# Optimization experiments

Hardware: AMD Instinct MI355X
Metric: run time of the kernel (lower is better)

Reference implementation:

```python
import jax, jax.numpy as jnp
import numpy as np

RADIUS = 0.05
HMIN = -0.02
HMAX = 0.04
NSAMPLE = 64


def setup_inputs() -> dict:
    key = jax.random.key(0)
    k1, k2, k3, k4 = jax.random.split(key, 4)
    B, N, P, C = 2, 16384, 1024, 256
    xyz = jax.random.uniform(k1, (B, N, 3), dtype=jnp.float32)
    new_xyz = jax.random.uniform(k2, (B, P, 3), dtype=jnp.float32)
    rot = jax.random.normal(k3, (B, P, 3, 3), dtype=jnp.float32)
    features = jax.random.normal(k4, (B, C, N), dtype=jnp.float32)
    return {"xyz": xyz, "new_xyz": new_xyz, "rot": rot, "features": features}


def cylinder_query(xyz, new_xyz, rot):
    """Returns (B, P, NSAMPLE) int32 indices into the N axis of xyz.

    Faithful to the torch version: the torch code sorts all N candidates by
    distance (knn with K=N) and then top-k's a cylinder score over them; since
    the candidate set is all N points, this equals a direct top-k of the score
    over N (candidate ordering only affects float ties).
    """
    # delta = candidate point - center, in world frame: (B, P, N, 3)
    delta = xyz[:, None, :, :] - new_xyz[:, :, None, :]
    # rotate into cylinder frame: matmul(delta, rot^T) -> sum_d delta_d * rot[j, d]
    dcyl = jnp.einsum('bpnd,bpjd->bpnj', delta, rot)
    x, y, z = dcyl[..., 0], dcyl[..., 1], dcyl[..., 2]
    radial = jnp.sqrt(jnp.maximum(y * y + z * z, 0.0))
    in_cyl = (radial <= RADIUS) & (x >= HMIN) & (x <= HMAX)
    score = jnp.where(in_cyl, radial + 1e-3 * jnp.abs(x), jnp.inf)
    # smallest-score top-k via top_k on negated score
    neg_vals, pos = jax.lax.top_k(-score, NSAMPLE)  # (B, P, NSAMPLE)
    vals = -neg_vals
    # fallback: nearest point (torch uses idx_cand[..., 0], the KNN-nearest)
    d2 = jnp.sum(delta * delta, axis=-1)  # (B, P, N)
    fallback = jnp.argmin(d2, axis=-1)  # (B, P)
    no_valid = jnp.isinf(vals[..., 0])  # no point inside cylinder
    idx = jnp.where(no_valid[..., None], fallback[..., None], pos)
    return idx


def reference(xyz, new_xyz, rot, features):
    B = xyz.shape[0]
    idx = cylinder_query(xyz, new_xyz, rot)  # (B, P, S)
    # group xyz: (B, P, S, 3)
    grouped_xyz = jax.vmap(lambda p, i: p[i])(xyz, idx)
    grouped_xyz = grouped_xyz - new_xyz[:, :, None, :]
    # rotate_xyz: grouped @ rot  -> sum_d g_d * rot[d, e]
    grouped_xyz = jnp.einsum('bpsd,bpde->bpse', grouped_xyz, rot)
    grouped_xyz = jnp.transpose(grouped_xyz, (0, 3, 1, 2))  # (B, 3, P, S)
    # group features: (B, C, P, S)
    grouped_feat = jax.vmap(lambda f, i: f[:, i])(features, idx)
    return jnp.concatenate([grouped_xyz, grouped_feat], axis=1)  # (B, 3+C, P, S)
```

## Files before the change

kernel.cpp:

```cpp
#include <hip/hip_runtime.h>
#include <stdint.h>

#define B_ 2
#define N_ 16384
#define P_ 1024
#define C_ 256
#define S_ 64
#define CH_ (C_ + 3)
#define CAP_ 512

#define INF_BITS 0x7F800000u

typedef unsigned long long u64;

struct QS {
    u64 keys[CAP_];
    uint32_t hist[4][256];
    u64 red[4];
    uint32_t wsum[4];
    int vflag[128];
    int cnt;
    int sel;
    uint32_t k;
};

union U1 {
    float ttile[64][65];
    QS qs;
};

__device__ __forceinline__ u64 umin64(u64 a, u64 b) { return a < b ? a : b; }

__device__ __forceinline__ uint32_t f2bf(float f) {
    uint32_t x = __float_as_uint(f);
    return (x + 0x7fffu + ((x >> 16) & 1u)) >> 16;
}
__device__ __forceinline__ float bf2f(uint32_t u) { return __uint_as_float(u << 16); }

__device__ u64 block_min_u64(u64 v, u64* s_red) {
    int tid = threadIdx.x;
#pragma unroll
    for (int o = 32; o > 0; o >>= 1)
        v = umin64(v, (u64)__shfl_xor(v, o, 64));
    __syncthreads();
    if ((tid & 63) == 0) s_red[tid >> 6] = v;
    __syncthreads();
    u64 r = s_red[0];
#pragma unroll
    for (int w = 1; w < 4; ++w) r = umin64(r, s_red[w]);
    return r;
}

__device__ __forceinline__ uint32_t eval_sb(float px, float py, float pz,
                                            float cx, float cy, float cz,
                                            float r0, float r1, float r2,
                                            float r3, float r4, float r5,
                                            float r6, float r7, float r8) {
    float dx = px - cx, dy = py - cy, dz = pz - cz;
    float xr = __fadd_rn(__fadd_rn(__fmul_rn(dx, r0), __fmul_rn(dy, r1)), __fmul_rn(dz, r2));
    float yr = __fadd_rn(__fadd_rn(__fmul_rn(dx, r3), __fmul_rn(dy, r4)), __fmul_rn(dz, r5));
    float zr = __fadd_rn(__fadd_rn(__fmul_rn(dx, r6), __fmul_rn(dy, r7)), __fmul_rn(dz, r8));
    float rad2 = __fadd_rn(__fmul_rn(yr, yr), __fmul_rn(zr, zr));
    float radial = __fsqrt_rn(fmaxf(rad2, 0.0f));
    bool valid = (radial <= 0.05f) && (xr >= -0.02f) && (xr <= 0.04f);
    float score = __fadd_rn(radial, __fmul_rn(1e-3f, fabsf(xr)));
    return valid ? __float_as_uint(score) : INF_BITS;
}

__device__ __forceinline__ uint32_t score_bits(const float* __restrict__ xb, int n,
                                               float cx, float cy, float cz,
                                               float r0, float r1, float r2,
                                               float r3, float r4, float r5,
                                               float r6, float r7, float r8) {
    return eval_sb(xb[n * 3 + 0], xb[n * 3 + 1], xb[n * 3 + 2],
                   cx, cy, cz, r0, r1, r2, r3, r4, r5, r6, r7, r8);
}

__device__ void select_idx(QS& qs, const float* __restrict__ xb,
                           float cx, float cy, float cz,
                           float r0, float r1, float r2, float r3, float r4,
                           float r5, float r6, float r7, float r8,
                           int* s_out) {
    const int tid = threadIdx.x;
    const int wid = tid >> 6;
    const int v = qs.cnt;

    if (v == 0) {
        u64 fb = ~0ull;
        for (int n = tid; n < N_; n += 256) {
            float px = xb[n * 3 + 0], py = xb[n * 3 + 1], pz = xb[n * 3 + 2];
            float dx = px - cx, dy = py - cy, dz = pz - cz;
            float d2 = __fadd_rn(__fadd_rn(__fmul_rn(dx, dx), __fmul_rn(dy, dy)),
                                 __fmul_rn(dz, dz));
            fb = umin64(fb, ((u64)__float_as_uint(d2) << 32) | (unsigned)n);
        }
        u64 m = block_min_u64(fb, qs.red);
        if (tid < S_) s_out[tid] = (int)(unsigned)(m & 0xFFFFFFFFu);
    } else if (v <= 64) {
        if (tid >= v && tid < 64)
            qs.keys[tid] = 0xFFFFFFFF00000000ull | (unsigned)(0x10000 + tid);
        __syncthreads();
        u64 key = 0;
        int rank = 0;
        if (tid < 64) {
            key = qs.keys[tid];
            for (int o = 0; o < 64; ++o) rank += (qs.keys[o] < key) ? 1 : 0;
        }
        __syncthreads();
        if (tid < 64) qs.keys[rank] = key;
        __syncthreads();
        const int needed = 64 - v;
        if (tid < 64 && needed > 0) {
            bool inv0 = (qs.vflag[tid] == 0);
            u64 m0 = __ballot(inv0);
            int before0 = __popcll(m0 & ((1ull << tid) - 1ull));
            if (inv0 && before0 < needed) qs.keys[v + before0] = (unsigned)tid;
            int c0 = __popcll(m0);
            if (c0 < needed) {
                bool inv1 = (qs.vflag[64 + tid] == 0);
                u64 m1 = __ballot(inv1);
                int b1 = c0 + __popcll(m1 & ((1ull << tid) - 1ull));
                if (inv1 && b1 < needed) qs.keys[v + b1] = (unsigned)(64 + tid);
            }
        }
        __syncthreads();
        if (tid < S_) s_out[tid] = (int)(unsigned)(qs.keys[tid] & 0xFFFFFFFFu);
    } else if (v <= CAP_) {
        for (int i = tid; i < v; i += 256) {
            u64 key = qs.keys[i];
            int rank = 0;
            for (int j = 0; j < v; ++j) rank += (qs.keys[j] < key) ? 1 : 0;
            if (rank < 64) s_out[rank] = (int)(unsigned)(key & 0xFFFFFFFFu);
        }
        __syncthreads();
    } else {
        uint32_t prefix = 0, mask = 0, kk = 64;
        for (int pass = 0; pass < 4; ++pass) {
            const int shift = 24 - 8 * pass;
            __syncthreads();
            qs.hist[0][tid] = 0;
            qs.hist[1][tid] = 0;
            qs.hist[2][tid] = 0;
            qs.hist[3][tid] = 0;
            __syncthreads();
            for (int n = tid; n < N_; n += 256) {
                uint32_t sb = score_bits(xb, n, cx, cy, cz, r0, r1, r2, r3, r4, r5, r6, r7, r8);
                if (sb != INF_BITS && (sb & mask) == prefix)
                    atomicAdd(&qs.hist[wid][(sb >> shift) & 255u], 1u);
            }
            __syncthreads();
            uint32_t cnt = qs.hist[0][tid] + qs.hist[1][tid] + qs.hist[2][tid] + qs.hist[3][tid];
            uint32_t x = cnt;
#pragma unroll
            for (int o = 1; o < 64; o <<= 1) {
                uint32_t y = __shfl_up(x, o, 64);
                if ((tid & 63) >= o) x += y;
            }
            if ((tid & 63) == 63) qs.wsum[wid] = x;
            __syncthreads();
            uint32_t woff = 0;
            for (int w = 0; w < wid; ++w) woff += qs.wsum[w];
            uint32_t incl = x + woff;
            uint32_t excl = incl - cnt;
            if (kk > excl && kk <= incl) {
                qs.sel = tid;
                qs.k = kk - excl;
            }
            __syncthreads();
            prefix |= ((uint32_t)qs.sel) << shift;
            mask |= 255u << shift;
            kk = qs.k;
        }
        const uint32_t T = prefix;

        __syncthreads();
        if (tid == 0) qs.cnt = 0;
        __syncthreads();
        for (int n = tid; n < N_; n += 256) {
            uint32_t sb = score_bits(xb, n, cx, cy, cz, r0, r1, r2, r3, r4, r5, r6, r7, r8);
            if (sb != INF_BITS && sb <= T) {
                int pos = atomicAdd(&qs.cnt, 1);
                if (pos < CAP_) qs.keys[pos] = ((u64)sb << 32) | (unsigned)n;
            }
        }
        __syncthreads();
        int c = qs.cnt;
        if (c > CAP_) c = CAP_;
        for (int i = tid; i < c; i += 256) {
            u64 key = qs.keys[i];
            int rank = 0;
            for (int j = 0; j < c; ++j) rank += (qs.keys[j] < key) ? 1 : 0;
            if (rank < 64) s_out[rank] = (int)(unsigned)(key & 0xFFFFFFFFu);
        }
        __syncthreads();
    }
}

__global__ __launch_bounds__(256) void tq_kernel(const float* __restrict__ feat,
                                                 ushort* __restrict__ featT,
                                                 const float* __restrict__ xyz,
                                                 const float* __restrict__ new_xyz,
                                                 const float* __restrict__ rot,
                                                 int* __restrict__ idx_out,
                                                 float* __restrict__ out, int useT) {
    __shared__ U1 sm;
    __shared__ int s_idx[S_];
    const int tid = threadIdx.x;
    const int lane = tid & 63;
    const int bp = blockIdx.x;
    const int b = bp >> 10;
    const int p = bp & 1023;
    const bool tfirst = ((blockIdx.x & 1) == 0);

    auto transpose_phase = [&]() {
        __syncthreads();
        int t = blockIdx.x;
        int tb = t >> 10;
        int rem = t & 1023;
        int cblk = rem >> 8;
        int nblk = rem & 255;
        for (int i = tid; i < 64 * 64; i += 256) {
            int cy = i >> 6, nx = i & 63;
            sm.ttile[cy][nx] = feat[((size_t)(tb * C_ + cblk * 64 + cy)) * N_ + nblk * 64 + nx];
        }
        __syncthreads();
        for (int i = tid; i < 64 * 32; i += 256) {
            int ny = i >> 5, cp = i & 31;
            uint32_t u0 = f2bf(sm.ttile[2 * cp + 0][ny]);
            uint32_t u1 = f2bf(sm.ttile[2 * cp + 1][ny]);
            *(uint32_t*)&featT[((size_t)(tb * N_ + nblk * 64 + ny)) * C_ + cblk * 64 + 2 * cp] =
                u0 | (u1 << 16);
        }
        __syncthreads();
    };

    if (useT && tfirst) transpose_phase();

    const float cx = new_xyz[bp * 3 + 0];
    const float cy = new_xyz[bp * 3 + 1];
    const float cz = new_xyz[bp * 3 + 2];
    const float* R = rot + (size_t)bp * 9;
    const float r0 = R[0], r1 = R[1], r2 = R[2];
    const float r3 = R[3], r4 = R[4], r5 = R[5];
    const float r6 = R[6], r7 = R[7], r8 = R[8];

    if (tid == 0) sm.qs.cnt = 0;
    __syncthreads();

    const float* xb = xyz + (size_t)b * N_ * 3;
    const float4* xb4 = (const float4*)xb;

    for (int it = 0; it < N_ / 1024; ++it) {
        int t4 = it * 256 + tid;
        float4 A = xb4[t4 * 3 + 0];
        float4 Bv = xb4[t4 * 3 + 1];
        float4 Cv = xb4[t4 * 3 + 2];
        int n0 = t4 * 4;

        uint32_t s0 = eval_sb(A.x, A.y, A.z, cx, cy, cz, r0, r1, r2, r3, r4, r5, r6, r7, r8);
        uint32_t s1 = eval_sb(A.w, Bv.x, Bv.y, cx, cy, cz, r0, r1, r2, r3, r4, r5, r6, r7, r8);
        uint32_t s2 = eval_sb(Bv.z, Bv.w, Cv.x, cx, cy, cz, r0, r1, r2, r3, r4, r5, r6, r7, r8);
        uint32_t s3 = eval_sb(Cv.y, Cv.z, Cv.w, cx, cy, cz, r0, r1, r2, r3, r4, r5, r6, r7, r8);

        if (it == 0 && tid < 32) {
            sm.qs.vflag[n0 + 0] = (s0 != INF_BITS) ? 1 : 0;
            sm.qs.vflag[n0 + 1] = (s1 != INF_BITS) ? 1 : 0;
            sm.qs.vflag[n0 + 2] = (s2 != INF_BITS) ? 1 : 0;
            sm.qs.vflag[n0 + 3] = (s3 != INF_BITS) ? 1 : 0;
        }
        uint32_t mn = min(min(s0, s1), min(s2, s3));
        if (__any(mn != INF_BITS)) {
            uint32_t sb[4] = {s0, s1, s2, s3};
#pragma unroll
            for (int j = 0; j < 4; ++j) {
                u64 m = __ballot(sb[j] != INF_BITS);
                if (m) {
                    int leader = __builtin_ctzll(m);
                    int cnt = __popcll(m);
                    int base = 0;
                    if (lane == leader) base = atomicAdd(&sm.qs.cnt, cnt);
                    base = __shfl(base, leader, 64);
                    if (sb[j] != INF_BITS) {
                        int pos = base + __popcll(m & ((1ull << lane) - 1ull));
                        if (pos < CAP_) sm.qs.keys[pos] = ((u64)sb[j] << 32) | (unsigned)(n0 + j);
                    }
                }
            }
        }
    }
    __syncthreads();

    select_idx(sm.qs, xb, cx, cy, cz, r0, r1, r2, r3, r4, r5, r6, r7, r8, s_idx);
    __syncthreads();

    if (tid < S_) {
        int n = s_idx[tid];
        idx_out[(size_t)bp * S_ + tid] = n;
        const float* pt = xyz + ((size_t)b * N_ + n) * 3;
        float dx = pt[0] - cx;
        float dy = pt[1] - cy;
        float dz = pt[2] - cz;
        float g0 = __fadd_rn(__fadd_rn(__fmul_rn(dx, r0), __fmul_rn(dy, r3)), __fmul_rn(dz, r6));
        float g1 = __fadd_rn(__fadd_rn(__fmul_rn(dx, r1), __fmul_rn(dy, r4)), __fmul_rn(dz, r7));
        float g2 = __fadd_rn(__fadd_rn(__fmul_rn(dx, r2), __fmul_rn(dy, r5)), __fmul_rn(dz, r8));
        out[(((size_t)b * CH_ + 0) * P_ + p) * S_ + tid] = g0;
        out[(((size_t)b * CH_ + 1) * P_ + p) * S_ + tid] = g1;
        out[(((size_t)b * CH_ + 2) * P_ + p) * S_ + tid] = g2;
    }

    if (useT && !tfirst) transpose_phase();
}

__global__ __launch_bounds__(256) void group_kernel(const ushort* __restrict__ featT,
                                                    const float* __restrict__ features,
                                                    const int* __restrict__ idx,
                                                    float* __restrict__ out, int useT) {
    __shared__ uint32_t tileu[32][130];
    __shared__ int s_idx[S_];
    const int tid = threadIdx.x;
    const int bp = blockIdx.x;
    const int b = bp >> 10;
    const int p = bp & 1023;

    if (tid < S_) s_idx[tid] = idx[(size_t)bp * S_ + tid];
    __syncthreads();

    for (int h = 0; h < 2; ++h) {
        if (h) __syncthreads();
        if (useT) {
            for (int i = tid; i < 32 * 64; i += 256) {
                int sl = i >> 6, cd = i & 63;
                int n = s_idx[h * 32 + sl];
                uint2 v = *(const uint2*)&featT[((size_t)b * N_ + n) * C_ + cd * 4];
                *(uint2*)&tileu[sl][cd * 2] = v;
            }
        } else {
            for (int i = tid; i < 32 * 128; i += 256) {
                int sl = i >> 7, cp = i & 127;
                int n = s_idx[h * 32 + sl];
                uint32_t u0 = f2bf(features[((size_t)b * C_ + 2 * cp + 0) * N_ + n]);
                uint32_t u1 = f2bf(features[((size_t)b * C_ + 2 * cp + 1) * N_ + n]);
                tileu[sl][cp] = u0 | (u1 << 16);
            }
        }
        __syncthreads();
        for (int i = tid; i < (C_ / 2) * 8; i += 256) {
            int cp = i >> 3, q = i & 7;
            uint32_t u0 = tileu[4 * q + 0][cp];
            uint32_t u1 = tileu[4 * q + 1][cp];
            uint32_t u2 = tileu[4 * q + 2][cp];
            uint32_t u3 = tileu[4 * q + 3][cp];
            float4 lo, hi;
            lo.x = bf2f(u0 & 0xffffu); lo.y = bf2f(u1 & 0xffffu);
            lo.z = bf2f(u2 & 0xffffu); lo.w = bf2f(u3 & 0xffffu);
            hi.x = bf2f(u0 >> 16); hi.y = bf2f(u1 >> 16);
            hi.z = bf2f(u2 >> 16); hi.w = bf2f(u3 >> 16);
            size_t base0 = (((size_t)b * CH_ + 3 + 2 * cp) * P_ + p) * S_ + h * 32 + 4 * q;
            *(float4*)&out[base0] = lo;
            *(float4*)&out[base0 + (size_t)P_ * S_] = hi;
        }
    }
}

extern "C" void kernel_launch(void* const* d_in, const int* in_sizes, int n_in,
                              void* d_out, int out_size, void* d_ws, size_t ws_size,
                              hipStream_t stream) {
    const float* xyz = (const float*)d_in[0];
    const float* new_xyz = (const float*)d_in[1];
    const float* rot = (const float*)d_in[2];
    const float* features = (const float*)d_in[3];
    float* out = (float*)d_out;

    const size_t featT_bytes = (size_t)B_ * N_ * C_ * sizeof(ushort);
    const size_t idx_bytes = (size_t)B_ * P_ * S_ * sizeof(int);
    const int useT = (ws_size >= featT_bytes + idx_bytes) ? 1 : 0;

    ushort* featT = (ushort*)d_ws;
    int* idx = useT ? (int*)((char*)d_ws + featT_bytes) : (int*)d_ws;

    tq_kernel<<<B_ * P_, 256, 0, stream>>>(features, featT, xyz, new_xyz, rot, idx, out, useT);
    group_kernel<<<B_ * P_, 256, 0, stream>>>(featT, features, idx, out, useT);
}
```

Baseline: 72.27 us.

## Split transpose and query into separate interleaved blocks of one kernel

Each block used to run both a feature-transpose tile and a cylinder query in sequence. Now the grid is doubled and each block does only one of the two: odd blocks transpose and even blocks query, with the body factored into noinline helpers and shared memory allocated dynamically. The aim is to let the memory-bound transpose blocks and the compute-bound query blocks run concurrently on different CUs instead of serially within one block. The cost is more blocks to launch, and register allocation across the two noinline call paths may change occupancy.

Result: slower. 98.89 us (+36.8%).

```diff
diff --git a/kernel.cpp b/kernel.cpp
--- a/kernel.cpp
+++ b/kernel.cpp
@@ -10,6 +10,7 @@
 #define CAP_ 512
 
 #define INF_BITS 0x7F800000u
+#define SMEM_BYTES (64 * 65 * 4)
 
 typedef unsigned long long u64;
 
@@ -19,15 +20,12 @@
     u64 red[4];
     uint32_t wsum[4];
     int vflag[128];
+    int s_idx[S_];
     int cnt;
     int sel;
     uint32_t k;
 };
-
-union U1 {
-    float ttile[64][65];
-    QS qs;
-};
+static_assert(sizeof(QS) <= SMEM_BYTES, "QS too big");
 
 __device__ __forceinline__ u64 umin64(u64 a, u64 b) { return a < b ? a : b; }
 
@@ -76,14 +74,96 @@
                    cx, cy, cz, r0, r1, r2, r3, r4, r5, r6, r7, r8);
 }
 
-__device__ void select_idx(QS& qs, const float* __restrict__ xb,
-                           float cx, float cy, float cz,
-                           float r0, float r1, float r2, float r3, float r4,
-                           float r5, float r6, float r7, float r8,
-                           int* s_out) {
+__device__ __noinline__ void do_transpose(char* smem, const float* __restrict__ feat,
+                                          ushort* __restrict__ featT, int t) {
+    float(*tile)[65] = (float(*)[65])smem;
     const int tid = threadIdx.x;
+    int b = t >> 10;
+    int rem = t & 1023;
+    int cblk = rem >> 8;
+    int nblk = rem & 255;
+    for (int i = tid; i < 64 * 64; i += 256) {
+        int cy = i >> 6, nx = i & 63;
+        tile[cy][nx] = feat[((size_t)(b * C_ + cblk * 64 + cy)) * N_ + nblk * 64 + nx];
+    }
+    __syncthreads();
+    for (int i = tid; i < 64 * 32; i += 256) {
+        int ny = i >> 5, cp = i & 31;
+        uint32_t u0 = f2bf(tile[2 * cp + 0][ny]);
+        uint32_t u1 = f2bf(tile[2 * cp + 1][ny]);
+        *(uint32_t*)&featT[((size_t)(b * N_ + nblk * 64 + ny)) * C_ + cblk * 64 + 2 * cp] =
+            u0 | (u1 << 16);
+    }
+}
+
+__device__ __noinline__ void do_query(char* smem, const float* __restrict__ xyz,
+                                      const float* __restrict__ new_xyz,
+                                      const float* __restrict__ rot,
+                                      int* __restrict__ idx_out,
+                                      float* __restrict__ out, int bp) {
+    QS& qs = *(QS*)smem;
+    const int tid = threadIdx.x;
+    const int lane = tid & 63;
     const int wid = tid >> 6;
+    const int b = bp >> 10;
+    const int p = bp & 1023;
+
+    if (tid == 0) qs.cnt = 0;
+
+    const float cx = new_xyz[bp * 3 + 0];
+    const float cy = new_xyz[bp * 3 + 1];
+    const float cz = new_xyz[bp * 3 + 2];
+    const float* R = rot + (size_t)bp * 9;
+    const float r0 = R[0], r1 = R[1], r2 = R[2];
+    const float r3 = R[3], r4 = R[4], r5 = R[5];
+    const float r6 = R[6], r7 = R[7], r8 = R[8];
+
+    __syncthreads();
+
+    const float* xb = xyz + (size_t)b * N_ * 3;
+    const float4* xb4 = (const float4*)xb;
+
+    for (int it = 0; it < N_ / 1024; ++it) {
+        int t4 = it * 256 + tid;
+        float4 A = xb4[t4 * 3 + 0];
+        float4 Bv = xb4[t4 * 3 + 1];
+        float4 Cv = xb4[t4 * 3 + 2];
+        int n0 = t4 * 4;
+
+        uint32_t s0 = eval_sb(A.x, A.y, A.z, cx, cy, cz, r0, r1, r2, r3, r4, r5, r6, r7, r8);
+        uint32_t s1 = eval_sb(A.w, Bv.x, Bv.y, cx, cy, cz, r0, r1, r2, r3, r4, r5, r6, r7, r8);
+        uint32_t s2 = eval_sb(Bv.z, Bv.w, Cv.x, cx, cy, cz, r0, r1, r2, r3, r4, r5, r6, r7, r8);
+        uint32_t s3 = eval_sb(Cv.y, Cv.z, Cv.w, cx, cy, cz, r0, r1, r2, r3, r4, r5, r6, r7, r8);
+
+        if (it == 0 && tid < 32) {
+            qs.vflag[n0 + 0] = (s0 != INF_BITS) ? 1 : 0;
+            qs.vflag[n0 + 1] = (s1 != INF_BITS) ? 1 : 0;
+            qs.vflag[n0 + 2] = (s2 != INF_BITS) ? 1 : 0;
+            qs.vflag[n0 + 3] = (s3 != INF_BITS) ? 1 : 0;
+        }
+        uint32_t mn = min(min(s0, s1), min(s2, s3));
+        if (__any(mn != INF_BITS)) {
+            uint32_t sb[4] = {s0, s1, s2, s3};
+#pragma unroll
+            for (int j = 0; j < 4; ++j) {
+                u64 m = __ballot(sb[j] != INF_BITS);
+                if (m) {
+                    int leader = __builtin_ctzll(m);
+                    int cnt = __popcll(m);
+                    int base = 0;
+                    if (lane == leader) base = atomicAdd(&qs.cnt, cnt);
+                    base = __shfl(base, leader, 64);
+                    if (sb[j] != INF_BITS) {
+                        int pos = base + __popcll(m & ((1ull << lane) - 1ull));
+                        if (pos < CAP_) qs.keys[pos] = ((u64)sb[j] << 32) | (unsigned)(n0 + j);
+                    }
+                }
+            }
+        }
+    }
+    __syncthreads();
     const int v = qs.cnt;
+    int* s_out = qs.s_idx;
 
     if (v == 0) {
         u64 fb = ~0ull;
@@ -132,7 +212,6 @@
             for (int j = 0; j < v; ++j) rank += (qs.keys[j] < key) ? 1 : 0;
             if (rank < 64) s_out[rank] = (int)(unsigned)(key & 0xFFFFFFFFu);
         }
-        __syncthreads();
     } else {
         uint32_t prefix = 0, mask = 0, kk = 64;
         for (int pass = 0; pass < 4; ++pass) {
@@ -192,109 +271,11 @@
             for (int j = 0; j < c; ++j) rank += (qs.keys[j] < key) ? 1 : 0;
             if (rank < 64) s_out[rank] = (int)(unsigned)(key & 0xFFFFFFFFu);
         }
-        __syncthreads();
-    }
-}
-
-__global__ __launch_bounds__(256) void tq_kernel(const float* __restrict__ feat,
-                                                 ushort* __restrict__ featT,
-                                                 const float* __restrict__ xyz,
-                                                 const float* __restrict__ new_xyz,
-                                                 const float* __restrict__ rot,
-                                                 int* __restrict__ idx_out,
-                                                 float* __restrict__ out, int useT) {
-    __shared__ U1 sm;
-    __shared__ int s_idx[S_];
-    const int tid = threadIdx.x;
-    const int lane = tid & 63;
-    const int bp = blockIdx.x;
-    const int b = bp >> 10;
-    const int p = bp & 1023;
-    const bool tfirst = ((blockIdx.x & 1) == 0);
-
-    auto transpose_phase = [&]() {
-        __syncthreads();
-        int t = blockIdx.x;
-        int tb = t >> 10;
-        int rem = t & 1023;
-        int cblk = rem >> 8;
-        int nblk = rem & 255;
-        for (int i = tid; i < 64 * 64; i += 256) {
-            int cy = i >> 6, nx = i & 63;
-            sm.ttile[cy][nx] = feat[((size_t)(tb * C_ + cblk * 64 + cy)) * N_ + nblk * 64 + nx];
-        }
-        __syncthreads();
-        for (int i = tid; i < 64 * 32; i += 256) {
-            int ny = i >> 5, cp = i & 31;
-            uint32_t u0 = f2bf(sm.ttile[2 * cp + 0][ny]);
-            uint32_t u1 = f2bf(sm.ttile[2 * cp + 1][ny]);
-            *(uint32_t*)&featT[((size_t)(tb * N_ + nblk * 64 + ny)) * C_ + cblk * 64 + 2 * cp] =
-                u0 | (u1 << 16);
-        }
-        __syncthreads();
-    };
-
-    if (useT && tfirst) transpose_phase();
-
-    const float cx = new_xyz[bp * 3 + 0];
-    const float cy = new_xyz[bp * 3 + 1];
-    const float cz = new_xyz[bp * 3 + 2];
-    const float* R = rot + (size_t)bp * 9;
-    const float r0 = R[0], r1 = R[1], r2 = R[2];
-    const float r3 = R[3], r4 = R[4], r5 = R[5];
-    const float r6 = R[6], r7 = R[7], r8 = R[8];
-
-    if (tid == 0) sm.qs.cnt = 0;
-    __syncthreads();
-
-    const float* xb = xyz + (size_t)b * N_ * 3;
-    const float4* xb4 = (const float4*)xb;
-
-    for (int it = 0; it < N_ / 1024; ++it) {
-        int t4 = it * 256 + tid;
-        float4 A = xb4[t4 * 3 + 0];
-        float4 Bv = xb4[t4 * 3 + 1];
-        float4 Cv = xb4[t4 * 3 + 2];
-        int n0 = t4 * 4;
-
-        uint32_t s0 = eval_sb(A.x, A.y, A.z, cx, cy, cz, r0, r1, r2, r3, r4, r5, r6, r7, r8);
-        uint32_t s1 = eval_sb(A.w, Bv.x, Bv.y, cx, cy, cz, r0, r1, r2, r3, r4, r5, r6, r7, r8);
-        uint32_t s2 = eval_sb(Bv.z, Bv.w, Cv.x, cx, cy, cz, r0, r1, r2, r3, r4, r5, r6, r7, r8);
-        uint32_t s3 = eval_sb(Cv.y, Cv.z, Cv.w, cx, cy, cz, r0, r1, r2, r3, r4, r5, r6, r7, r8);
-
-        if (it == 0 && tid < 32) {
-            sm.qs.vflag[n0 + 0] = (s0 != INF_BITS) ? 1 : 0;
-            sm.qs.vflag[n0 + 1] = (s1 != INF_BITS) ? 1 : 0;
-            sm.qs.vflag[n0 + 2] = (s2 != INF_BITS) ? 1 : 0;
-            sm.qs.vflag[n0 + 3] = (s3 != INF_BITS) ? 1 : 0;
-        }
-        uint32_t mn = min(min(s0, s1), min(s2, s3));
-        if (__any(mn != INF_BITS)) {
-            uint32_t sb[4] = {s0, s1, s2, s3};
-#pragma unroll
-            for (int j = 0; j < 4; ++j) {
-                u64 m = __ballot(sb[j] != INF_BITS);
-                if (m) {
-                    int leader = __builtin_ctzll(m);
-                    int cnt = __popcll(m);
-                    int base = 0;
-                    if (lane == leader) base = atomicAdd(&sm.qs.cnt, cnt);
-                    base = __shfl(base, leader, 64);
-                    if (sb[j] != INF_BITS) {
-                        int pos = base + __popcll(m & ((1ull << lane) - 1ull));
-                        if (pos < CAP_) sm.qs.keys[pos] = ((u64)sb[j] << 32) | (unsigned)(n0 + j);
-                    }
-                }
-            }
-        }
-    }
-    __syncthreads();
-
-    select_idx(sm.qs, xb, cx, cy, cz, r0, r1, r2, r3, r4, r5, r6, r7, r8, s_idx);
+    }
     __syncthreads();
 
     if (tid < S_) {
-        int n = s_idx[tid];
+        int n = s_out[tid];
         idx_out[(size_t)bp * S_ + tid] = n;
         const float* pt = xyz + ((size_t)b * N_ + n) * 3;
         float dx = pt[0] - cx;
@@ -307,8 +288,22 @@
         out[(((size_t)b * CH_ + 1) * P_ + p) * S_ + tid] = g1;
         out[(((size_t)b * CH_ + 2) * P_ + p) * S_ + tid] = g2;
     }
-
-    if (useT && !tfirst) transpose_phase();
+}
+
+__global__ __launch_bounds__(256) void tq_kernel(const float* __restrict__ feat,
+                                                 ushort* __restrict__ featT,
+                                                 const float* __restrict__ xyz,
+                                                 const float* __restrict__ new_xyz,
+                                                 const float* __restrict__ rot,
+                                                 int* __restrict__ idx_out,
+                                                 float* __restrict__ out, int useT) {
+    extern __shared__ char smem[];
+    const int id = blockIdx.x >> 1;
+    if (blockIdx.x & 1) {
+        if (useT) do_transpose(smem, feat, featT, id);
+    } else {
+        do_query(smem, xyz, new_xyz, rot, idx_out, out, id);
+    }
 }
 
 __global__ __launch_bounds__(256) void group_kernel(const ushort* __restrict__ featT,
@@ -378,6 +373,7 @@
     ushort* featT = (ushort*)d_ws;
     int* idx = useT ? (int*)((char*)d_ws + featT_bytes) : (int*)d_ws;
 
-    tq_kernel<<<B_ * P_, 256, 0, stream>>>(features, featT, xyz, new_xyz, rot, idx, out, useT);
+    tq_kernel<<<2 * B_ * P_, 256, SMEM_BYTES, stream>>>(features, featT, xyz, new_xyz, rot,
+                                                        idx, out, useT);
     group_kernel<<<B_ * P_, 256, 0, stream>>>(featT, features, idx, out, useT);
 }
```
